# Kernel optimization log

Measured on AMD Instinct MI355X. Metric: run time of the kernel, lower is better.

## Reference

```python
import jax, jax.numpy as jnp
import numpy as np

NUM_EMBEDDINGS = 1024
EMBEDDING_DIM = 64
COMMITMENT_COST = 0.25


def setup_inputs() -> dict:
    key = jax.random.key(0)
    k1, k2 = jax.random.split(key)
    inputs = jax.random.normal(k1, (16, 4096, EMBEDDING_DIM), dtype=jnp.float32)
    # codebook initialized uniform(-1/K, 1/K) as in the torch module
    emb_weight = jax.random.uniform(
        k2, (NUM_EMBEDDINGS, EMBEDDING_DIM), dtype=jnp.float32,
        minval=-1.0 / NUM_EMBEDDINGS, maxval=1.0 / NUM_EMBEDDINGS)
    return {"inputs": inputs, "emb_weight": emb_weight}


def reference(inputs, emb_weight):
    B, T, D = inputs.shape
    flat = inputs.reshape(-1, D)  # [N, D]
    distances = (jnp.sum(flat * flat, axis=1, keepdims=True)
                 + jnp.sum(emb_weight * emb_weight, axis=1)
                 - 2.0 * jnp.matmul(flat, emb_weight.T))
    encoding_indices = jnp.argmin(distances, axis=1)  # [N]
    # one-hot @ codebook == direct gather
    quantized = emb_weight[encoding_indices]  # [N, D]
    q_latent_loss = jnp.mean((jax.lax.stop_gradient(quantized) - flat) ** 2)
    e_latent_loss = jnp.mean((quantized - jax.lax.stop_gradient(flat)) ** 2)
    loss = q_latent_loss + COMMITMENT_COST * e_latent_loss
    # straight-through estimator
    quantized_st = flat + jax.lax.stop_gradient(quantized - flat)
    quantized_st = quantized_st.reshape(B, T, D)
    return quantized_st, loss, encoding_indices[:, None]
```

## Files before the change

### kernel.cpp

```cpp
#include <hip/hip_runtime.h>

typedef float f4 __attribute__((ext_vector_type(4)));
typedef __attribute__((ext_vector_type(4))) float f32x4;
typedef __attribute__((ext_vector_type(8))) short bf16x8;

#define NV 65536
#define D 64
#define K 1024
#define NT 512
#define BM 128
#define TILE 256
#define MARGIN 4.0e-3f
#define CAP 32
#define LOSS_OFF 4194304
#define IDX_OFF  4194305

__device__ __forceinline__ unsigned f2bf(float f) {
  unsigned u = __builtin_bit_cast(unsigned, f);
  return (u + 0x7fffu + ((u >> 16) & 1u)) >> 16;
}

__global__ void vq_prep(const float* __restrict__ E, float* __restrict__ eSq,
                        float* __restrict__ loss) {
  int k = blockIdx.x * 256 + threadIdx.x;
  if (k == 0) *loss = 0.0f;
  if (k < K) {
    const float* row = E + (size_t)k * D;
    float r[8];
#pragma unroll
    for (int j = 0; j < 8; ++j) r[j] = __fmul_rn(row[j], row[j]);
#pragma unroll
    for (int i = 8; i < D; i += 8)
#pragma unroll
      for (int j = 0; j < 8; ++j)
        r[j] = __fadd_rn(r[j], __fmul_rn(row[i + j], row[i + j]));
    eSq[k] = __fadd_rn(
        __fadd_rn(__fadd_rn(r[0], r[1]), __fadd_rn(r[2], r[3])),
        __fadd_rn(__fadd_rn(r[4], r[5]), __fadd_rn(r[6], r[7])));
  }
}

__device__ __forceinline__ void stage_tile(const float* __restrict__ E,
                                           unsigned short* dstbase, int tile,
                                           int t) {
  const int rc = t >> 1, h = t & 1;
  const float* src = E + ((size_t)(tile * TILE + rc)) * D + h * 32;
  char* dst = reinterpret_cast<char*>(dstbase) + rc * 128;
  const int sw = (rc & 7) << 4;
#pragma unroll
  for (int s = 0; s < 4; ++s) {
    f4 a = *reinterpret_cast<const f4*>(src + s * 8);
    f4 b = *reinterpret_cast<const f4*>(src + s * 8 + 4);
    uint4 pk;
    pk.x = f2bf(a[0]) | (f2bf(a[1]) << 16);
    pk.y = f2bf(a[2]) | (f2bf(a[3]) << 16);
    pk.z = f2bf(b[0]) | (f2bf(b[1]) << 16);
    pk.w = f2bf(b[2]) | (f2bf(b[3]) << 16);
    *reinterpret_cast<uint4*>(dst + ((h * 64 + s * 16) ^ sw)) = pk;
  }
}

__device__ __forceinline__ bf16x8 ld_a(const float* p) {
  f4 a = *reinterpret_cast<const f4*>(p);
  f4 b = *reinterpret_cast<const f4*>(p + 4);
  bf16x8 r;
  r[0] = (short)f2bf(a[0]); r[1] = (short)f2bf(a[1]);
  r[2] = (short)f2bf(a[2]); r[3] = (short)f2bf(a[3]);
  r[4] = (short)f2bf(b[0]); r[5] = (short)f2bf(b[1]);
  r[6] = (short)f2bf(b[2]); r[7] = (short)f2bf(b[3]);
  return r;
}

__global__ __launch_bounds__(NT, 4) void vq_main(
    const float* __restrict__ X, const float* __restrict__ E,
    const float* __restrict__ eSq, float* __restrict__ out) {
  __shared__ unsigned short EbfL[TILE * 64];
  __shared__ float eSqL[K];
  __shared__ unsigned cntL[BM];
  __shared__ unsigned short candL[BM * CAP];
  __shared__ int sidxL[BM];

  const int t = threadIdx.x;
  const int lane = t & 63;
  const int w = t >> 6;
  const int l15 = lane & 15, l4 = lane >> 4;
  const int bv0 = blockIdx.x * BM;

  const float* xv = X + (size_t)(bv0 + w * 16 + l15) * D;
  bf16x8 a0 = ld_a(xv + l4 * 8);
  bf16x8 a1 = ld_a(xv + 32 + l4 * 8);

#pragma unroll
  for (int i = 0; i < 2; ++i) eSqL[t + NT * i] = eSq[t + NT * i];
  if (t < BM) cntL[t] = 0;

  float umin[4];
#pragma unroll
  for (int r = 0; r < 4; ++r) umin[r] = 3.4e38f;
  const char* eB = reinterpret_cast<const char*>(EbfL);

  for (int tile = 0; tile < 4; ++tile) {
    __syncthreads();
    stage_tile(E, EbfL, tile, t);
    __syncthreads();
#pragma unroll 4
    for (int ct = 0; ct < 16; ++ct) {
      const int lr = ct * 16 + l15;
      const int rsw = (lr & 7) << 4;
      bf16x8 b0 = *reinterpret_cast<const bf16x8*>(eB + lr * 128 + ((l4 * 16) ^ rsw));
      bf16x8 b1 = *reinterpret_cast<const bf16x8*>(eB + lr * 128 + ((64 + l4 * 16) ^ rsw));
      f32x4 acc = {0.f, 0.f, 0.f, 0.f};
      acc = __builtin_amdgcn_mfma_f32_16x16x32_bf16(a0, b0, acc, 0, 0, 0);
      acc = __builtin_amdgcn_mfma_f32_16x16x32_bf16(a1, b1, acc, 0, 0, 0);
      const float ee = eSqL[tile * TILE + lr];
#pragma unroll
      for (int r = 0; r < 4; ++r)
        umin[r] = fminf(umin[r], __fmaf_rn(-2.0f, acc[r], ee));
    }
  }
  float thr[4];
#pragma unroll
  for (int r = 0; r < 4; ++r) {
#pragma unroll
    for (int off = 1; off < 16; off <<= 1)
      umin[r] = fminf(umin[r], __shfl_xor(umin[r], off, 64));
    thr[r] = umin[r] + MARGIN;
  }

  for (int tile = 0; tile < 4; ++tile) {
    __syncthreads();
    stage_tile(E, EbfL, tile, t);
    __syncthreads();
#pragma unroll 4
    for (int ct = 0; ct < 16; ++ct) {
      const int lr = ct * 16 + l15;
      const int rsw = (lr & 7) << 4;
      bf16x8 b0 = *reinterpret_cast<const bf16x8*>(eB + lr * 128 + ((l4 * 16) ^ rsw));
      bf16x8 b1 = *reinterpret_cast<const bf16x8*>(eB + lr * 128 + ((64 + l4 * 16) ^ rsw));
      f32x4 acc = {0.f, 0.f, 0.f, 0.f};
      acc = __builtin_amdgcn_mfma_f32_16x16x32_bf16(a0, b0, acc, 0, 0, 0);
      acc = __builtin_amdgcn_mfma_f32_16x16x32_bf16(a1, b1, acc, 0, 0, 0);
      const int gc = tile * TILE + lr;
      const float ee = eSqL[gc];
#pragma unroll
      for (int r = 0; r < 4; ++r) {
        if (__fmaf_rn(-2.0f, acc[r], ee) <= thr[r]) {
          const int v = w * 16 + l4 * 4 + r;
          const unsigned pos = atomicAdd(&cntL[v], 1u);
          if (pos < CAP) candL[v * CAP + pos] = (unsigned short)gc;
        }
      }
    }
  }
  __syncthreads();

  {
    const int v = t >> 2, par = t & 3;
    const int gv = bv0 + v;
    const float* xr = X + (size_t)gv * D;
    float rr[8];
#pragma unroll
    for (int j = 0; j < 8; ++j) rr[j] = __fmul_rn(xr[j], xr[j]);
#pragma unroll
    for (int i = 8; i < 64; i += 8)
#pragma unroll
      for (int j = 0; j < 8; ++j)
        rr[j] = __fadd_rn(rr[j], __fmul_rn(xr[i + j], xr[i + j]));
    const float xx = __fadd_rn(
        __fadd_rn(__fadd_rn(rr[0], rr[1]), __fadd_rn(rr[2], rr[3])),
        __fadd_rn(__fadd_rn(rr[4], rr[5]), __fadd_rn(rr[6], rr[7])));

    float best = 3.4e38f;
    int bi = 0x7fffffff;
    const unsigned n = cntL[v];
    if (n <= CAP) {
      for (unsigned i = par; i < n; i += 4) {
        const int c = candL[v * CAP + i];
        const float* er = E + (size_t)c * D;
        float m = 0.f;
#pragma unroll
        for (int j = 0; j < 64; ++j) m = fmaf(er[j], xr[j], m);
        const float dd = __fsub_rn(__fadd_rn(xx, eSqL[c]), 2.0f * m);
        if (dd < best || (dd == best && c < bi)) { best = dd; bi = c; }
      }
    } else {
      for (int c = par; c < K; c += 4) {
        const float* er = E + (size_t)c * D;
        float m = 0.f;
#pragma unroll
        for (int j = 0; j < 64; ++j) m = fmaf(er[j], xr[j], m);
        const float dd = __fsub_rn(__fadd_rn(xx, eSqL[c]), 2.0f * m);
        if (dd < best || (dd == best && c < bi)) { best = dd; bi = c; }
      }
    }
#pragma unroll
    for (int off = 1; off < 4; off <<= 1) {
      const float ov = __shfl_xor(best, off, 64);
      const int oi = __shfl_xor(bi, off, 64);
      if (ov < best || (ov == best && oi < bi)) { best = ov; bi = oi; }
    }
    if (par == 0) sidxL[v] = bi;
  }
  __syncthreads();

  {
    const int v = t >> 2, h = t & 3;
    const int gv = bv0 + v;
    const int code = sidxL[v];
    const f4* er = reinterpret_cast<const f4*>(E + (size_t)code * D + h * 16);
    const f4* xr = reinterpret_cast<const f4*>(X + (size_t)gv * D + h * 16);
    f4* op = reinterpret_cast<f4*>(out + (size_t)gv * D + h * 16);
    float lsum = 0.f;
#pragma unroll
    for (int i = 0; i < 4; ++i) {
      f4 e4 = er[i], x4 = xr[i];
      float d0 = e4[0] - x4[0], d1 = e4[1] - x4[1];
      float d2 = e4[2] - x4[2], d3 = e4[3] - x4[3];
      lsum += d0 * d0 + d1 * d1 + d2 * d2 + d3 * d3;
      op[i] = e4;
    }
    if (t < BM) out[IDX_OFF + bv0 + t] = (float)sidxL[t];
#pragma unroll
    for (int off = 1; off < 64; off <<= 1) lsum += __shfl_xor(lsum, off, 64);
    if (lane == 0)
      atomicAdd(out + LOSS_OFF, lsum * (1.25f / (float)(NV * (size_t)D)));
  }
}

extern "C" void kernel_launch(void* const* d_in, const int* in_sizes, int n_in,
                              void* d_out, int out_size, void* d_ws, size_t ws_size,
                              hipStream_t stream) {
  const float* X = (const float*)d_in[0];
  const float* E = (const float*)d_in[1];
  float* out = (float*)d_out;
  float* eSq = (float*)d_ws;
  vq_prep<<<4, 256, 0, stream>>>(E, eSq, out + LOSS_OFF);
  vq_main<<<NV / BM, NT, 0, stream>>>(X, E, eSq, out);
}
```

Measured before the change: 111.8 us.

## Pre-convert codebook to MFMA-fragment bf16 layout in prep kernel, drop LDS staging

The prep kernel now also converts the codebook to bf16 once, stored in workspace in the exact per-lane MFMA B-fragment order. The main kernel reads B fragments directly from global memory/L2 instead of restaging and converting the codebook into LDS per block, twice per block. This removes the tile loop and its barriers. Blocks shrink to 256 threads and 64 rows, doubling the grid. The trade-off is heavier reliance on L2 bandwidth for the codebook reads.

```diff
diff --git a/kernel.cpp b/kernel.cpp
--- a/kernel.cpp
+++ b/kernel.cpp
@@ -7,9 +7,7 @@
 #define NV 65536
 #define D 64
 #define K 1024
-#define NT 512
-#define BM 128
-#define TILE 256
+#define BM 64
 #define MARGIN 4.0e-3f
 #define CAP 32
 #define LOSS_OFF 4194304
@@ -20,12 +18,13 @@
   return (u + 0x7fffu + ((u >> 16) & 1u)) >> 16;
 }
 
-__global__ void vq_prep(const float* __restrict__ E, float* __restrict__ eSq,
+__global__ void vq_prep(const float* __restrict__ E, float* __restrict__ ws,
                         float* __restrict__ loss) {
-  int k = blockIdx.x * 256 + threadIdx.x;
-  if (k == 0) *loss = 0.0f;
-  if (k < K) {
-    const float* row = E + (size_t)k * D;
+  const int n = blockIdx.x * 256 + threadIdx.x;
+  unsigned short* Ebf = reinterpret_cast<unsigned short*>(ws + K);
+  if (n == 0) *loss = 0.0f;
+  if (n < K) {
+    const float* row = E + (size_t)n * D;
     float r[8];
 #pragma unroll
     for (int j = 0; j < 8; ++j) r[j] = __fmul_rn(row[j], row[j]);
@@ -34,30 +33,23 @@
 #pragma unroll
       for (int j = 0; j < 8; ++j)
         r[j] = __fadd_rn(r[j], __fmul_rn(row[i + j], row[i + j]));
-    eSq[k] = __fadd_rn(
+    ws[n] = __fadd_rn(
         __fadd_rn(__fadd_rn(r[0], r[1]), __fadd_rn(r[2], r[3])),
         __fadd_rn(__fadd_rn(r[4], r[5]), __fadd_rn(r[6], r[7])));
   }
-}
-
-__device__ __forceinline__ void stage_tile(const float* __restrict__ E,
-                                           unsigned short* dstbase, int tile,
-                                           int t) {
-  const int rc = t >> 1, h = t & 1;
-  const float* src = E + ((size_t)(tile * TILE + rc)) * D + h * 32;
-  char* dst = reinterpret_cast<char*>(dstbase) + rc * 128;
-  const int sw = (rc & 7) << 4;
-#pragma unroll
-  for (int s = 0; s < 4; ++s) {
-    f4 a = *reinterpret_cast<const f4*>(src + s * 8);
-    f4 b = *reinterpret_cast<const f4*>(src + s * 8 + 4);
-    uint4 pk;
-    pk.x = f2bf(a[0]) | (f2bf(a[1]) << 16);
-    pk.y = f2bf(a[2]) | (f2bf(a[3]) << 16);
-    pk.z = f2bf(b[0]) | (f2bf(b[1]) << 16);
-    pk.w = f2bf(b[2]) | (f2bf(b[3]) << 16);
-    *reinterpret_cast<uint4*>(dst + ((h * 64 + s * 16) ^ sw)) = pk;
-  }
+  const int fi = n >> 6, lane = n & 63;
+  const int ct = fi >> 1, half = fi & 1;
+  const int code = ct * 16 + (lane & 15);
+  const int d0 = half * 32 + (lane >> 4) * 8;
+  const float* src = E + (size_t)code * D + d0;
+  f4 a = *reinterpret_cast<const f4*>(src);
+  f4 b = *reinterpret_cast<const f4*>(src + 4);
+  uint4 pk;
+  pk.x = f2bf(a[0]) | (f2bf(a[1]) << 16);
+  pk.y = f2bf(a[2]) | (f2bf(a[3]) << 16);
+  pk.z = f2bf(b[0]) | (f2bf(b[1]) << 16);
+  pk.w = f2bf(b[2]) | (f2bf(b[3]) << 16);
+  *reinterpret_cast<uint4*>(Ebf + (size_t)n * 8) = pk;
 }
 
 __device__ __forceinline__ bf16x8 ld_a(const float* p) {
@@ -71,14 +63,15 @@
   return r;
 }
 
-__global__ __launch_bounds__(NT, 4) void vq_main(
+__global__ __launch_bounds__(256, 2) void vq_main(
     const float* __restrict__ X, const float* __restrict__ E,
-    const float* __restrict__ eSq, float* __restrict__ out) {
-  __shared__ unsigned short EbfL[TILE * 64];
+    const float* __restrict__ ws, float* __restrict__ out) {
   __shared__ float eSqL[K];
   __shared__ unsigned cntL[BM];
   __shared__ unsigned short candL[BM * CAP];
   __shared__ int sidxL[BM];
+
+  const unsigned short* Ebf = reinterpret_cast<const unsigned short*>(ws + K);
 
   const int t = threadIdx.x;
   const int lane = t & 63;
@@ -91,32 +84,26 @@
   bf16x8 a1 = ld_a(xv + 32 + l4 * 8);
 
 #pragma unroll
-  for (int i = 0; i < 2; ++i) eSqL[t + NT * i] = eSq[t + NT * i];
+  for (int i = 0; i < 4; ++i) eSqL[t + 256 * i] = ws[t + 256 * i];
   if (t < BM) cntL[t] = 0;
+  __syncthreads();
+
+  const unsigned short* ebase = Ebf + (size_t)lane * 8;
 
   float umin[4];
 #pragma unroll
   for (int r = 0; r < 4; ++r) umin[r] = 3.4e38f;
-  const char* eB = reinterpret_cast<const char*>(EbfL);
-
-  for (int tile = 0; tile < 4; ++tile) {
-    __syncthreads();
-    stage_tile(E, EbfL, tile, t);
-    __syncthreads();
 #pragma unroll 4
-    for (int ct = 0; ct < 16; ++ct) {
-      const int lr = ct * 16 + l15;
-      const int rsw = (lr & 7) << 4;
-      bf16x8 b0 = *reinterpret_cast<const bf16x8*>(eB + lr * 128 + ((l4 * 16) ^ rsw));
-      bf16x8 b1 = *reinterpret_cast<const bf16x8*>(eB + lr * 128 + ((64 + l4 * 16) ^ rsw));
-      f32x4 acc = {0.f, 0.f, 0.f, 0.f};
-      acc = __builtin_amdgcn_mfma_f32_16x16x32_bf16(a0, b0, acc, 0, 0, 0);
-      acc = __builtin_amdgcn_mfma_f32_16x16x32_bf16(a1, b1, acc, 0, 0, 0);
-      const float ee = eSqL[tile * TILE + lr];
-#pragma unroll
-      for (int r = 0; r < 4; ++r)
-        umin[r] = fminf(umin[r], __fmaf_rn(-2.0f, acc[r], ee));
-    }
+  for (int ct = 0; ct < 64; ++ct) {
+    bf16x8 b0 = *reinterpret_cast<const bf16x8*>(ebase + ct * 1024);
+    bf16x8 b1 = *reinterpret_cast<const bf16x8*>(ebase + ct * 1024 + 512);
+    f32x4 acc = {0.f, 0.f, 0.f, 0.f};
+    acc = __builtin_amdgcn_mfma_f32_16x16x32_bf16(a0, b0, acc, 0, 0, 0);
+    acc = __builtin_amdgcn_mfma_f32_16x16x32_bf16(a1, b1, acc, 0, 0, 0);
+    const float ee = eSqL[ct * 16 + l15];
+#pragma unroll
+    for (int r = 0; r < 4; ++r)
+      umin[r] = fminf(umin[r], __fmaf_rn(-2.0f, acc[r], ee));
   }
   float thr[4];
 #pragma unroll
@@ -127,28 +114,21 @@
     thr[r] = umin[r] + MARGIN;
   }
 
-  for (int tile = 0; tile < 4; ++tile) {
-    __syncthreads();
-    stage_tile(E, EbfL, tile, t);
-    __syncthreads();
 #pragma unroll 4
-    for (int ct = 0; ct < 16; ++ct) {
-      const int lr = ct * 16 + l15;
-      const int rsw = (lr & 7) << 4;
-      bf16x8 b0 = *reinterpret_cast<const bf16x8*>(eB + lr * 128 + ((l4 * 16) ^ rsw));
-      bf16x8 b1 = *reinterpret_cast<const bf16x8*>(eB + lr * 128 + ((64 + l4 * 16) ^ rsw));
-      f32x4 acc = {0.f, 0.f, 0.f, 0.f};
-      acc = __builtin_amdgcn_mfma_f32_16x16x32_bf16(a0, b0, acc, 0, 0, 0);
-      acc = __builtin_amdgcn_mfma_f32_16x16x32_bf16(a1, b1, acc, 0, 0, 0);
-      const int gc = tile * TILE + lr;
-      const float ee = eSqL[gc];
-#pragma unroll
-      for (int r = 0; r < 4; ++r) {
-        if (__fmaf_rn(-2.0f, acc[r], ee) <= thr[r]) {
-          const int v = w * 16 + l4 * 4 + r;
-          const unsigned pos = atomicAdd(&cntL[v], 1u);
-          if (pos < CAP) candL[v * CAP + pos] = (unsigned short)gc;
-        }
+  for (int ct = 0; ct < 64; ++ct) {
+    bf16x8 b0 = *reinterpret_cast<const bf16x8*>(ebase + ct * 1024);
+    bf16x8 b1 = *reinterpret_cast<const bf16x8*>(ebase + ct * 1024 + 512);
+    f32x4 acc = {0.f, 0.f, 0.f, 0.f};
+    acc = __builtin_amdgcn_mfma_f32_16x16x32_bf16(a0, b0, acc, 0, 0, 0);
+    acc = __builtin_amdgcn_mfma_f32_16x16x32_bf16(a1, b1, acc, 0, 0, 0);
+    const int gc = ct * 16 + l15;
+    const float ee = eSqL[gc];
+#pragma unroll
+    for (int r = 0; r < 4; ++r) {
+      if (__fmaf_rn(-2.0f, acc[r], ee) <= thr[r]) {
+        const int v = w * 16 + l4 * 4 + r;
+        const unsigned pos = atomicAdd(&cntL[v], 1u);
+        if (pos < CAP) candL[v * CAP + pos] = (unsigned short)gc;
       }
     }
   }
@@ -233,7 +213,7 @@
   const float* X = (const float*)d_in[0];
   const float* E = (const float*)d_in[1];
   float* out = (float*)d_out;
-  float* eSq = (float*)d_ws;
-  vq_prep<<<4, 256, 0, stream>>>(E, eSq, out + LOSS_OFF);
-  vq_main<<<NV / BM, NT, 0, stream>>>(X, E, eSq, out);
-}
+  float* ws = (float*)d_ws;
+  vq_prep<<<32, 256, 0, stream>>>(E, ws, out + LOSS_OFF);
+  vq_main<<<NV / BM, 256, 0, stream>>>(X, E, ws, out);
+}
```

After: 105.8 us. 5.3% less time.
